# Kernel optimization log

Hardware: AMD Instinct MI355X
Metric: run time of the kernel (lower is better)

The kernel has to match this reference:

```python
import jax, jax.numpy as jnp
import numpy as np

B, C, T, F = 4, 96, 320, 256
BN_EPS = 1e-5


def _cbp(x, W, b, gamma, beta, mean, var, a):
    """1x1 Conv2d + BatchNorm2d (inference stats) + PReLU (single param)."""
    y = jnp.einsum('oc,bctf->botf', W, x) + b[None, :, None, None]
    scale = gamma * jax.lax.rsqrt(var + BN_EPS)
    y = (y - mean[None, :, None, None]) * scale[None, :, None, None] + beta[None, :, None, None]
    return jnp.where(y >= 0, y, a * y)


def setup_inputs() -> dict:
    key = jax.random.key(0)
    ks = jax.random.split(key, 24)
    d = {"inp": jax.random.normal(ks[0], (B, C, T, F), dtype=jnp.float32)}

    def mk_params(i, cout):
        kk = jax.random.split(ks[i], 7)
        return dict(
            W=jax.random.normal(kk[0], (cout, C), dtype=jnp.float32) / np.sqrt(C),
            b=jnp.zeros((cout,), dtype=jnp.float32),
            gamma=jnp.ones((cout,), dtype=jnp.float32) + 0.1 * jax.random.normal(kk[1], (cout,), dtype=jnp.float32),
            beta=0.1 * jax.random.normal(kk[2], (cout,), dtype=jnp.float32),
            mean=0.1 * jax.random.normal(kk[3], (cout,), dtype=jnp.float32),
            var=jax.random.uniform(kk[4], (cout,), dtype=jnp.float32) + 0.5,
            a=jnp.float32(0.25),
        )

    for tag, i, cout in (("f", 1, 3 * C), ("t", 2, 2 * C), ("p", 3, C)):
        p = mk_params(i, cout)
        for k, v in p.items():
            d[k + "_" + tag] = v
    return d


def reference(inp,
              W_f, b_f, gamma_f, beta_f, mean_f, var_f, a_f,
              W_t, b_t, gamma_t, beta_t, mean_t, var_t, a_t,
              W_p, b_p, gamma_p, beta_p, mean_p, var_p, a_p):
    c = inp.shape[1]
    scale = 1.0 / jnp.sqrt(jnp.float32(c))

    # frequency-axis attention
    f_qkv = _cbp(inp, W_f, b_f, gamma_f, beta_f, mean_f, var_f, a_f)  # [B,3C,T,F]
    qf, kf, v = f_qkv[:, :c], f_qkv[:, c:2 * c], f_qkv[:, 2 * c:]
    f_score = jnp.einsum('bctf,bcty->btfy', qf, kf) * scale
    f_score = jax.nn.softmax(f_score, axis=-1)
    f_out = jnp.einsum('btfy,bcty->bctf', f_score, v)

    # time-axis attention (NOTE: original's masked_fill is non-inplace and
    # its result is discarded, so the causal mask has NO effect; replicated.)
    t_qk = _cbp(inp, W_t, b_t, gamma_t, beta_t, mean_t, var_t, a_t)  # [B,2C,T,F]
    qt, kt = t_qk[:, :c], t_qk[:, c:]
    t_score = jnp.einsum('bctf,bcyf->bfty', qt, kt) * scale
    t_score = jax.nn.softmax(t_score, axis=-1)
    t_out = jnp.einsum('bfty,bcyf->bctf', t_score, f_out)

    out = _cbp(t_out, W_p, b_p, gamma_p, beta_p, mean_p, var_p, a_p)
    return out + inp
```

## Files before the change

### kernel.cpp

```cpp
#include <hip/hip_runtime.h>
#include <math.h>

typedef float f4 __attribute__((ext_vector_type(4)));
typedef float f2 __attribute__((ext_vector_type(2)));
typedef float f32x4 __attribute__((ext_vector_type(4)));
typedef _Float16 h8 __attribute__((ext_vector_type(8)));

constexpr int B_ = 4, C_ = 96, T_ = 320, F_ = 256;
constexpr int TF_ = T_ * F_;
constexpr float EPS_ = 1e-5f;
constexpr size_t QH_ = (size_t)C_ * TF_;

constexpr int WHF = 0, WLF = 27648, WHT = 55296, WLT = 73728,
              WHP = 92160, WLP = 101376, WTOT = 110592;

__global__ __launch_bounds__(256)
void prep_kernel(const float* __restrict__ Wf, const float* __restrict__ Wt,
                 const float* __restrict__ Wp,
                 const float* __restrict__ bf, const float* __restrict__ gf,
                 const float* __restrict__ bef, const float* __restrict__ mf,
                 const float* __restrict__ vf,
                 const float* __restrict__ bt, const float* __restrict__ gt,
                 const float* __restrict__ bet, const float* __restrict__ mt,
                 const float* __restrict__ vt,
                 const float* __restrict__ bp, const float* __restrict__ gp,
                 const float* __restrict__ bep, const float* __restrict__ mp,
                 const float* __restrict__ vp,
                 _Float16* __restrict__ wsp, float* __restrict__ scsh)
{
    const int gtid = blockIdx.x * 256 + threadIdx.x;
    const int gsz  = gridDim.x * 256;
    for (int i = gtid; i < 27648; i += gsz) {
        const float w = Wf[i]; const _Float16 h = (_Float16)w;
        wsp[WHF + i] = h; wsp[WLF + i] = (_Float16)(w - (float)h);
    }
    for (int i = gtid; i < 18432; i += gsz) {
        const float w = Wt[i]; const _Float16 h = (_Float16)w;
        wsp[WHT + i] = h; wsp[WLT + i] = (_Float16)(w - (float)h);
    }
    for (int i = gtid; i < 9216; i += gsz) {
        const float w = Wp[i]; const _Float16 h = (_Float16)w;
        wsp[WHP + i] = h; wsp[WLP + i] = (_Float16)(w - (float)h);
    }
    if (gtid < 288) {
        const float sc = gf[gtid] * rsqrtf(vf[gtid] + EPS_);
        scsh[2 * gtid] = sc;
        scsh[2 * gtid + 1] = fmaf(bf[gtid] - mf[gtid], sc, bef[gtid]);
    } else if (gtid < 480) {
        const int i = gtid - 288;
        const float sc = gt[i] * rsqrtf(vt[i] + EPS_);
        scsh[576 + 2 * i] = sc;
        scsh[576 + 2 * i + 1] = fmaf(bt[i] - mt[i], sc, bet[i]);
    } else if (gtid < 576) {
        const int i = gtid - 480;
        const float sc = gp[i] * rsqrtf(vp[i] + EPS_);
        scsh[960 + 2 * i] = sc;
        scsh[960 + 2 * i + 1] = fmaf(bp[i] - mp[i], sc, bep[i]);
    }
}

__global__ __launch_bounds__(256, 3)
void conv_ft(const float* __restrict__ x, const _Float16* __restrict__ wsp,
             const float* __restrict__ scsh,
             const float* __restrict__ aPf, const float* __restrict__ aPt,
             _Float16* __restrict__ yf, _Float16* __restrict__ yt,
             int bsx, int bsyf, int bsyt)
{
    constexpr int LS = 200;
    extern __shared__ _Float16 ldsh[];
    _Float16* Xs0 = ldsh;
    _Float16* Xs1 = ldsh + 64 * LS;

    x  += (size_t)blockIdx.y * bsx;
    yf += (size_t)blockIdx.y * bsyf;
    yt += (size_t)blockIdx.y * bsyt;

    const int tid = threadIdx.x;
    const int p0A = blockIdx.x * 128;
    const int p0B = p0A + 64;

    {
        const float* xg = x + p0A;
        for (int e = tid; e < 64 * 12; e += 256) {
            const int p = e & 63, k0 = (e >> 6) * 8;
            const float* xp = xg + (size_t)k0 * TF_ + p;
            h8 hv, lv;
#pragma unroll
            for (int j = 0; j < 8; ++j) {
                const float xv = xp[(size_t)j * TF_];
                const _Float16 xh = (_Float16)xv;
                hv[j] = xh;
                lv[j] = (_Float16)(xv - (float)xh);
            }
            *(h8*)&Xs0[p * LS + k0]      = hv;
            *(h8*)&Xs0[p * LS + 96 + k0] = lv;
        }
    }

    const int lane = tid & 63, wid = tid >> 6;
    const int l16 = lane & 15, lg = lane >> 4;
    const int wm = wid >> 1, wn = wid & 1;
    const float af_ = aPf[0], at_ = aPt[0];
    __syncthreads();

    float xpre[3][8];
#pragma unroll
    for (int it = 0; it < 3; ++it) {
        const int e = tid + it * 256;
        const int p = e & 63, k0 = (e >> 6) * 8;
        const float* xp = x + p0B + (size_t)k0 * TF_ + p;
#pragma unroll
        for (int j = 0; j < 8; ++j) xpre[it][j] = xp[(size_t)j * TF_];
    }

    auto compute5 = [&](const _Float16* Xs, int p0) {
#pragma unroll 1
        for (int cg = 0; cg < 5; ++cg) {
            const _Float16 *Wh, *Wl; const float* ss; float a; _Float16* yo;
            if (cg < 3) {
                Wh = wsp + WHF + cg * 9216;  Wl = wsp + WLF + cg * 9216;
                ss = scsh + cg * 192;        a = af_;
                yo = yf + (size_t)cg * QH_;
            } else {
                const int c2 = cg - 3;
                Wh = wsp + WHT + c2 * 9216;  Wl = wsp + WLT + c2 * 9216;
                ss = scsh + 576 + c2 * 192;  a = at_;
                yo = yt + (size_t)c2 * QH_;
            }

            f32x4 acc[3][2];
#pragma unroll
            for (int m = 0; m < 3; ++m)
#pragma unroll
                for (int n = 0; n < 2; ++n) acc[m][n] = (f32x4){0.f, 0.f, 0.f, 0.f};

#pragma unroll
            for (int kk = 0; kk < 3; ++kk) {
                h8 bfh[2], bfl[2];
#pragma unroll
                for (int n = 0; n < 2; ++n) {
                    const int prow = (wn * 2 + n) * 16 + l16;
                    bfh[n] = *(const h8*)&Xs[prow * LS + kk * 32 + lg * 8];
                    bfl[n] = *(const h8*)&Xs[prow * LS + 96 + kk * 32 + lg * 8];
                }
#pragma unroll
                for (int m = 0; m < 3; ++m) {
                    const int row = (wm * 3 + m) * 16 + l16;
                    const h8 wh = *(const h8*)&Wh[row * 96 + kk * 32 + lg * 8];
                    const h8 wl = *(const h8*)&Wl[row * 96 + kk * 32 + lg * 8];
#pragma unroll
                    for (int n = 0; n < 2; ++n) {
                        acc[m][n] = __builtin_amdgcn_mfma_f32_16x16x32_f16(wh, bfh[n], acc[m][n], 0, 0, 0);
                        acc[m][n] = __builtin_amdgcn_mfma_f32_16x16x32_f16(wl, bfh[n], acc[m][n], 0, 0, 0);
                        acc[m][n] = __builtin_amdgcn_mfma_f32_16x16x32_f16(wh, bfl[n], acc[m][n], 0, 0, 0);
                    }
                }
            }

#pragma unroll
            for (int m = 0; m < 3; ++m) {
#pragma unroll
                for (int r = 0; r < 4; ++r) {
                    const int col = (wm * 3 + m) * 16 + lg * 4 + r;
                    const f2 sp = *(const f2*)&ss[2 * col];
                    _Float16* yr = yo + (size_t)col * TF_ + p0 + wn * 32 + l16;
#pragma unroll
                    for (int n = 0; n < 2; ++n) {
                        const float v = fmaf(acc[m][n][r], sp[0], sp[1]);
                        yr[n * 16] = (_Float16)(v >= 0.f ? v : a * v);
                    }
                }
            }
        }
    };

    compute5(Xs0, p0A);

#pragma unroll
    for (int it = 0; it < 3; ++it) {
        const int e = tid + it * 256;
        const int p = e & 63, k0 = (e >> 6) * 8;
        h8 hv, lv;
#pragma unroll
        for (int j = 0; j < 8; ++j) {
            const _Float16 xh = (_Float16)xpre[it][j];
            hv[j] = xh;
            lv[j] = (_Float16)(xpre[it][j] - (float)xh);
        }
        *(h8*)&Xs1[p * LS + k0]      = hv;
        *(h8*)&Xs1[p * LS + 96 + k0] = lv;
    }
    __syncthreads();

    compute5(Xs1, p0B);
}

__global__ __launch_bounds__(256, 3)
void conv_p(const _Float16* __restrict__ x, const _Float16* __restrict__ wsp,
            const float* __restrict__ scsh, const float* __restrict__ aPp,
            _Float16* __restrict__ y, int bsx, int bsy)
{
    constexpr int LS = 104, PT = 160, NN = 5;
    extern __shared__ _Float16 ldsh[];
    _Float16* Xs = ldsh;

    x += (size_t)blockIdx.y * bsx;
    y += (size_t)blockIdx.y * bsy;

    const int tid = threadIdx.x;
    const int pt  = blockIdx.x & 1;
    const int g   = blockIdx.x >> 1;
    const int p0  = pt * PT;

    const _Float16* xg = x + (size_t)g * 96 * T_ + p0;
    for (int e = tid; e < PT * 12; e += 256) {
        const int p = e % PT, k0 = (e / PT) * 8;
        const _Float16* xp = xg + (size_t)k0 * T_ + p;
        h8 hv;
#pragma unroll
        for (int j = 0; j < 8; ++j) hv[j] = xp[(size_t)j * T_];
        *(h8*)&Xs[p * LS + k0] = hv;
    }

    const int lane = tid & 63, wid = tid >> 6;
    const int l16 = lane & 15, lg = lane >> 4;
    const int wm = wid >> 1, wn = wid & 1;
    const float a = aPp[0];
    const _Float16* Wh = wsp + WHP;
    const _Float16* Wl = wsp + WLP;
    const float* ss = scsh + 960;
    __syncthreads();

    f32x4 acc[3][NN];
#pragma unroll
    for (int m = 0; m < 3; ++m)
#pragma unroll
        for (int n = 0; n < NN; ++n) acc[m][n] = (f32x4){0.f, 0.f, 0.f, 0.f};

#pragma unroll
    for (int kk = 0; kk < 3; ++kk) {
        h8 bf[NN];
#pragma unroll
        for (int n = 0; n < NN; ++n)
            bf[n] = *(const h8*)&Xs[((wn * NN + n) * 16 + l16) * LS + kk * 32 + lg * 8];
#pragma unroll
        for (int m = 0; m < 3; ++m) {
            const int row = (wm * 3 + m) * 16 + l16;
            const h8 wh = *(const h8*)&Wh[row * 96 + kk * 32 + lg * 8];
            const h8 wl = *(const h8*)&Wl[row * 96 + kk * 32 + lg * 8];
#pragma unroll
            for (int n = 0; n < NN; ++n) {
                acc[m][n] = __builtin_amdgcn_mfma_f32_16x16x32_f16(wh, bf[n], acc[m][n], 0, 0, 0);
                acc[m][n] = __builtin_amdgcn_mfma_f32_16x16x32_f16(wl, bf[n], acc[m][n], 0, 0, 0);
            }
        }
    }

#pragma unroll
    for (int m = 0; m < 3; ++m) {
#pragma unroll
        for (int r = 0; r < 4; ++r) {
            const int col = (wm * 3 + m) * 16 + lg * 4 + r;
            const f2 sp = *(const f2*)&ss[2 * col];
            _Float16* yr = y + ((size_t)g * 96 + col) * T_ + p0 + wn * NN * 16 + l16;
#pragma unroll
            for (int n = 0; n < NN; ++n) {
                const float v = fmaf(acc[m][n][r], sp[0], sp[1]);
                yr[n * 16] = (_Float16)(v >= 0.f ? v : a * v);
            }
        }
    }
}

__device__ __forceinline__ void tr64_body(const _Float16* __restrict__ in,
                                          _Float16* __restrict__ out,
                                          int Mo, int No, int n0, int m0,
                                          _Float16* tile)
{
    const int t = threadIdx.x, ty = t >> 3, tx8 = t & 7;
#pragma unroll
    for (int r = 0; r < 2; ++r) {
        const int n = ty + r * 32;
        const h8 v = *(const h8*)&in[(size_t)(n0 + n) * Mo + m0 + tx8 * 8];
        const int c = tx8 ^ (n >> 3);
        *(h8*)&tile[n * 72 + c * 8] = v;
    }
    __syncthreads();
#pragma unroll
    for (int r = 0; r < 2; ++r) {
        const int mt = ty + r * 32;
        h8 v;
#pragma unroll
        for (int j = 0; j < 8; ++j) {
            const int n = tx8 * 8 + j;
            const int c = (mt >> 3) ^ tx8;
            v[j] = tile[n * 72 + c * 8 + (mt & 7)];
        }
        *(h8*)&out[(size_t)(m0 + mt) * No + n0 + tx8 * 8] = v;
    }
}

__global__ __launch_bounds__(256)
void transpose_trA(const _Float16* __restrict__ doh, _Float16* __restrict__ wsh)
{
    __shared__ _Float16 tile[64 * 72];
    const int b = blockIdx.z >> 1, t = blockIdx.z & 1;
    const _Float16* in  = t ? doh + (size_t)b * 2 * QH_
                            : wsh + (size_t)b * 3 * QH_;
    _Float16*       out = t ? wsh + (size_t)b * 3 * QH_ + 2 * QH_
                            : wsh + (size_t)b * 3 * QH_ + QH_;
    tr64_body(in, out, F_, C_ * T_, blockIdx.x * 64, blockIdx.y * 64, tile);
}

__global__ __launch_bounds__(256)
void transpose_trB(const _Float16* __restrict__ doh, _Float16* __restrict__ wsh)
{
    __shared__ _Float16 tile[64 * 72];
    const int b = blockIdx.z;
    tr64_body(doh + (size_t)b * 2 * QH_ + QH_, wsh + (size_t)b * 3 * QH_,
              F_, C_ * T_, blockIdx.x * 64, blockIdx.y * 64, tile);
}

__global__ __launch_bounds__(256)
void transpose_hf_res(const _Float16* __restrict__ in, const float* __restrict__ res,
                      float* __restrict__ out, int si, int sr, int so)
{
    __shared__ _Float16 tile[64 * 72];
    in  += (size_t)blockIdx.z * si;
    res += (size_t)blockIdx.z * sr;
    out += (size_t)blockIdx.z * so;
    const int n0 = blockIdx.x * 64, m0 = blockIdx.y * 64;
    const int t = threadIdx.x, ty = t >> 3, tx8 = t & 7;
#pragma unroll
    for (int r = 0; r < 2; ++r) {
        const int n = ty + r * 32;
        const h8 v = *(const h8*)&in[(size_t)(n0 + n) * (C_ * T_) + m0 + tx8 * 8];
        const int c = tx8 ^ (n >> 3);
        *(h8*)&tile[n * 72 + c * 8] = v;
    }
    __syncthreads();
#pragma unroll
    for (int r = 0; r < 2; ++r) {
        const int mt = ty + r * 32;
        const size_t obase = (size_t)(m0 + mt) * F_ + n0 + tx8 * 8;
        const f4 r0 = *(const f4*)&res[obase];
        const f4 r1 = *(const f4*)&res[obase + 4];
        f4 o0, o1;
#pragma unroll
        for (int j = 0; j < 8; ++j) {
            const int n = tx8 * 8 + j;
            const int c = (mt >> 3) ^ tx8;
            const float v = (float)tile[n * 72 + c * 8 + (mt & 7)];
            if (j < 4) o0[j] = v + r0[j]; else o1[j - 4] = v + r1[j - 4];
        }
        *(f4*)&out[obase]     = o0;
        *(f4*)&out[obase + 4] = o1;
    }
}

template<int MODE>
__global__ __launch_bounds__(256, 2)
void attn_mfma(const _Float16* __restrict__ Qb, const _Float16* __restrict__ Kb,
               const _Float16* __restrict__ Vb, _Float16* __restrict__ Ob,
               int qs, int ks, int vs, int os)
{
    constexpr int NY  = (MODE == 0) ? 256 : 320;
    constexpr int LD  = (MODE == 0) ? TF_ : T_;
    constexpr int NT  = NY / 16;
    constexpr int NYK = NY / 32;
    constexpr int KS  = 104;
    constexpr int VPS = NY + 24;
    constexpr int KVH = (NY * KS > 96 * VPS) ? NY * KS : 96 * VPS;
    constexpr int NG  = (MODE == 0) ? T_ : F_;
    constexpr int GOFF = (MODE == 0) ? F_ : C_ * T_;

    extern __shared__ _Float16 ldsh[];
    _Float16* KV = ldsh;
    _Float16* Pw = ldsh + KVH;

    const int lb    = blockIdx.y;
    const int strip = blockIdx.x / NG;
    const int grp   = blockIdx.x % NG;
    const int m0    = strip * 64;
    const size_t off = (size_t)grp * GOFF;
    const _Float16* Q = Qb + (size_t)lb * qs + off;
    const _Float16* K = Kb + (size_t)lb * ks + off;
    const _Float16* V = Vb + (size_t)lb * vs + off;
    _Float16*       O = Ob + (size_t)lb * os + off;

    const int tid  = threadIdx.x;
    const int lane = tid & 63, wid = tid >> 6;
    const int l16  = lane & 15, lg = lane >> 4;
    const int mw   = wid * 16;
    const float scale = 0.10206207261596575f;

    for (int e = tid; e < NY * 12; e += 256) {
        const int yy = e % NY, k0 = (e / NY) * 8;
        const _Float16* kp = K + (size_t)k0 * LD + yy;
        h8 hv;
#pragma unroll
        for (int j = 0; j < 8; ++j) hv[j] = kp[(size_t)j * LD];
        *(h8*)&KV[yy * KS + k0] = hv;
    }

    h8 aQ[3];
#pragma unroll
    for (int kk = 0; kk < 3; ++kk) {
        const _Float16* qp = Q + (size_t)(kk * 32 + lg * 8) * LD + m0 + mw + l16;
#pragma unroll
        for (int j = 0; j < 8; ++j) aQ[kk][j] = qp[(size_t)j * LD];
    }
    __syncthreads();

    f32x4 sacc[NT];
#pragma unroll
    for (int t = 0; t < NT; ++t) sacc[t] = (f32x4){0.f, 0.f, 0.f, 0.f};
#pragma unroll
    for (int kk = 0; kk < 3; ++kk) {
#pragma unroll
        for (int t = 0; t < NT; ++t) {
            const h8 bK = *(const h8*)&KV[(t * 16 + l16) * KS + kk * 32 + lg * 8];
            sacc[t] = __builtin_amdgcn_mfma_f32_16x16x32_f16(aQ[kk], bK, sacc[t], 0, 0, 0);
        }
    }

#pragma unroll
    for (int r = 0; r < 4; ++r) {
        float mx = sacc[0][r];
#pragma unroll
        for (int t = 1; t < NT; ++t) mx = fmaxf(mx, sacc[t][r]);
        for (int d = 1; d < 16; d <<= 1) mx = fmaxf(mx, __shfl_xor(mx, d));
        float pv[NT];
        float sum = 0.f;
#pragma unroll
        for (int t = 0; t < NT; ++t) {
            pv[t] = __expf((sacc[t][r] - mx) * scale); sum += pv[t];
        }
        for (int d = 1; d < 16; d <<= 1) sum += __shfl_xor(sum, d);
        const float inv = 1.f / sum;
#pragma unroll
        for (int t = 0; t < NT; ++t) sacc[t][r] = pv[t] * inv;
    }
    __syncthreads();

    constexpr int NY8 = NY / 8;
    for (int e = tid; e < 96 * NY8; e += 256) {
        const int c = e / NY8, y8 = e - c * NY8;
        *(h8*)&KV[c * VPS + y8 * 8] = *(const h8*)(V + (size_t)c * LD + y8 * 8);
    }
    __syncthreads();

    _Float16* Pme = Pw + wid * 640;
    f32x4 oacc[6];
#pragma unroll
    for (int ct = 0; ct < 6; ++ct) oacc[ct] = (f32x4){0.f, 0.f, 0.f, 0.f};

#pragma unroll
    for (int yk = 0; yk < NYK; ++yk) {
#pragma unroll
        for (int h = 0; h < 2; ++h)
#pragma unroll
            for (int r = 0; r < 4; ++r)
                Pme[(lg * 4 + r) * 40 + h * 16 + l16] = (_Float16)sacc[2 * yk + h][r];
        const h8 pf = *(const h8*)&Pme[l16 * 40 + lg * 8];
#pragma unroll
        for (int ct = 0; ct < 6; ++ct) {
            const h8 av = *(const h8*)&KV[(ct * 16 + l16) * VPS + yk * 32 + lg * 8];
            oacc[ct] = __builtin_amdgcn_mfma_f32_16x16x32_f16(av, pf, oacc[ct], 0, 0, 0);
        }
    }
#pragma unroll
    for (int ct = 0; ct < 6; ++ct)
#pragma unroll
        for (int r = 0; r < 4; ++r)
            O[(size_t)(ct * 16 + lg * 4 + r) * LD + m0 + mw + l16] = (_Float16)oacc[ct][r];
}

extern "C" void kernel_launch(void* const* d_in, const int* in_sizes, int n_in,
                              void* d_out, int out_size, void* d_ws, size_t ws_size,
                              hipStream_t stream)
{
    const float* inp = (const float*)d_in[0];
    const float* W_f = (const float*)d_in[1];  const float* b_f = (const float*)d_in[2];
    const float* g_f = (const float*)d_in[3];  const float* be_f = (const float*)d_in[4];
    const float* m_f = (const float*)d_in[5];  const float* v_f = (const float*)d_in[6];
    const float* a_f = (const float*)d_in[7];
    const float* W_t = (const float*)d_in[8];  const float* b_t = (const float*)d_in[9];
    const float* g_t = (const float*)d_in[10]; const float* be_t = (const float*)d_in[11];
    const float* m_t = (const float*)d_in[12]; const float* v_t = (const float*)d_in[13];
    const float* a_t = (const float*)d_in[14];
    const float* W_p = (const float*)d_in[15]; const float* b_p = (const float*)d_in[16];
    const float* g_p = (const float*)d_in[17]; const float* be_p = (const float*)d_in[18];
    const float* m_p = (const float*)d_in[19]; const float* v_p = (const float*)d_in[20];
    const float* a_p = (const float*)d_in[21];

    hipFuncSetAttribute((const void*)conv_ft,
                        hipFuncAttributeMaxDynamicSharedMemorySize, 51200);
    hipFuncSetAttribute((const void*)conv_p,
                        hipFuncAttributeMaxDynamicSharedMemorySize, 33280);
    hipFuncSetAttribute((const void*)attn_mfma<0>,
                        hipFuncAttributeMaxDynamicSharedMemorySize, 58880);
    hipFuncSetAttribute((const void*)attn_mfma<1>,
                        hipFuncAttributeMaxDynamicSharedMemorySize, 71680);

    constexpr int QH = (int)QH_;
    const size_t need4 = (size_t)12 * QH * 2 + (size_t)WTOT * 2 + 1152 * 4 + 4096;
    const int G = (ws_size >= need4) ? 4 : 2;

    _Float16* wsh  = (_Float16*)d_ws;
    _Float16* wsp  = wsh + (size_t)3 * G * QH;
    float*    scsh = (float*)(wsp + WTOT);

    prep_kernel<<<dim3(128), dim3(256), 0, stream>>>(
        W_f, W_t, W_p, b_f, g_f, be_f, m_f, v_f,
        b_t, g_t, be_t, m_t, v_t, b_p, g_p, be_p, m_p, v_p, wsp, scsh);

    for (int p = 0; p < B_ / G; ++p) {
        const float* xb  = inp + (size_t)p * G * QH;
        float*       dob = (float*)d_out + (size_t)p * G * QH;
        _Float16*    doh = (_Float16*)dob;

        conv_ft<<<dim3(640, G), dim3(256), 51200, stream>>>(
            xb, wsp, scsh, a_f, a_t, wsh, doh, QH, 3 * QH, 2 * QH);
        attn_mfma<0><<<dim3(T_ * (F_ / 64), G), dim3(256), 58880, stream>>>(
            wsh, wsh + QH_, wsh + 2 * QH_, wsh, 3 * QH, 3 * QH, 3 * QH, 3 * QH);
        transpose_trA<<<dim3(480, 4, 2 * G), dim3(256), 0, stream>>>(doh, wsh);
        transpose_trB<<<dim3(480, 4, G), dim3(256), 0, stream>>>(doh, wsh);
        attn_mfma<1><<<dim3(F_ * (T_ / 64), G), dim3(256), 71680, stream>>>(
            wsh + 2 * QH_, wsh, wsh + QH_, wsh + 2 * QH_,
            3 * QH, 3 * QH, 3 * QH, 3 * QH);
        conv_p<<<dim3(F_ * 2, G), dim3(256), 33280, stream>>>(
            wsh + 2 * QH_, wsp, scsh, a_p, wsh, 3 * QH, 3 * QH);
        transpose_hf_res<<<dim3(4, 480, G), dim3(256), 0, stream>>>(
            wsh, xb, dob, 3 * QH, QH, QH);
    }
}
```

Baseline: 713.7 us.

## Fuse time-axis attention with output 1x1 conv+BN+PReLU projection

Adds a fused kernel that runs the time-axis attention and then applies the projection conv (split-fp16 weights), BN scale/shift and PReLU straight from the attention output tile staged in shared memory. This removes the separate conv_p launch and the round trip of the attention output through global memory. It needs extra workspace (16 QH halves), and when that is not available it falls back to the old path. It also sets launch bounds of 2 blocks per CU with 70 KB of LDS, and adds register pressure from the epilogue.

```diff
diff --git a/kernel.cpp b/kernel.cpp
--- a/kernel.cpp
+++ b/kernel.cpp
@@ -476,6 +476,169 @@
             O[(size_t)(ct * 16 + lg * 4 + r) * LD + m0 + mw + l16] = (_Float16)oacc[ct][r];
 }
 
+__global__ __launch_bounds__(256, 2)
+void attn1_fused(const _Float16* __restrict__ Qb, const _Float16* __restrict__ Kb,
+                 const _Float16* __restrict__ Vb, _Float16* __restrict__ tmpb,
+                 const _Float16* __restrict__ wsp, const float* __restrict__ scsh,
+                 const float* __restrict__ aPp,
+                 int qs, int ks, int vs, int ts)
+{
+    constexpr int NY = 320, LD = T_, NT = 20, NYK = 10;
+    constexpr int KS = 104, VPS = 344;
+    constexpr int KVH = NY * KS;
+    constexpr int OS  = 104;
+
+    extern __shared__ _Float16 ldsh[];
+    _Float16* KV = ldsh;
+    _Float16* Pw = ldsh + KVH;
+    _Float16* Ot = ldsh;
+
+    const int lb    = blockIdx.y;
+    const int strip = blockIdx.x / F_;
+    const int grp   = blockIdx.x % F_;
+    const int m0    = strip * 64;
+    const size_t off = (size_t)grp * (C_ * T_);
+    const _Float16* Q = Qb + (size_t)lb * qs + off;
+    const _Float16* K = Kb + (size_t)lb * ks + off;
+    const _Float16* V = Vb + (size_t)lb * vs + off;
+    _Float16*     tmp = tmpb + (size_t)lb * ts + (size_t)grp * (96 * T_);
+
+    const int tid  = threadIdx.x;
+    const int lane = tid & 63, wid = tid >> 6;
+    const int l16  = lane & 15, lg = lane >> 4;
+    const int mw   = wid * 16;
+    const float scale = 0.10206207261596575f;
+
+    for (int e = tid; e < NY * 12; e += 256) {
+        const int yy = e % NY, k0 = (e / NY) * 8;
+        const _Float16* kp = K + (size_t)k0 * LD + yy;
+        h8 hv;
+#pragma unroll
+        for (int j = 0; j < 8; ++j) hv[j] = kp[(size_t)j * LD];
+        *(h8*)&KV[yy * KS + k0] = hv;
+    }
+
+    h8 aQ[3];
+#pragma unroll
+    for (int kk = 0; kk < 3; ++kk) {
+        const _Float16* qp = Q + (size_t)(kk * 32 + lg * 8) * LD + m0 + mw + l16;
+#pragma unroll
+        for (int j = 0; j < 8; ++j) aQ[kk][j] = qp[(size_t)j * LD];
+    }
+    __syncthreads();
+
+    f32x4 sacc[NT];
+#pragma unroll
+    for (int t = 0; t < NT; ++t) sacc[t] = (f32x4){0.f, 0.f, 0.f, 0.f};
+#pragma unroll
+    for (int kk = 0; kk < 3; ++kk) {
+#pragma unroll
+        for (int t = 0; t < NT; ++t) {
+            const h8 bK = *(const h8*)&KV[(t * 16 + l16) * KS + kk * 32 + lg * 8];
+            sacc[t] = __builtin_amdgcn_mfma_f32_16x16x32_f16(aQ[kk], bK, sacc[t], 0, 0, 0);
+        }
+    }
+
+#pragma unroll
+    for (int r = 0; r < 4; ++r) {
+        float mx = sacc[0][r];
+#pragma unroll
+        for (int t = 1; t < NT; ++t) mx = fmaxf(mx, sacc[t][r]);
+        for (int d = 1; d < 16; d <<= 1) mx = fmaxf(mx, __shfl_xor(mx, d));
+        float pv[NT];
+        float sum = 0.f;
+#pragma unroll
+        for (int t = 0; t < NT; ++t) {
+            pv[t] = __expf((sacc[t][r] - mx) * scale); sum += pv[t];
+        }
+        for (int d = 1; d < 16; d <<= 1) sum += __shfl_xor(sum, d);
+        const float inv = 1.f / sum;
+#pragma unroll
+        for (int t = 0; t < NT; ++t) sacc[t][r] = pv[t] * inv;
+    }
+    __syncthreads();
+
+    for (int e = tid; e < 96 * 40; e += 256) {
+        const int c = e / 40, y8 = e - c * 40;
+        *(h8*)&KV[c * VPS + y8 * 8] = *(const h8*)(V + (size_t)c * LD + y8 * 8);
+    }
+    __syncthreads();
+
+    _Float16* Pme = Pw + wid * 640;
+    f32x4 oacc[6];
+#pragma unroll
+    for (int ct = 0; ct < 6; ++ct) oacc[ct] = (f32x4){0.f, 0.f, 0.f, 0.f};
+
+#pragma unroll
+    for (int yk = 0; yk < NYK; ++yk) {
+#pragma unroll
+        for (int h = 0; h < 2; ++h)
+#pragma unroll
+            for (int r = 0; r < 4; ++r)
+                Pme[(lg * 4 + r) * 40 + h * 16 + l16] = (_Float16)sacc[2 * yk + h][r];
+        const h8 pf = *(const h8*)&Pme[l16 * 40 + lg * 8];
+#pragma unroll
+        for (int ct = 0; ct < 6; ++ct) {
+            const h8 av = *(const h8*)&KV[(ct * 16 + l16) * VPS + yk * 32 + lg * 8];
+            oacc[ct] = __builtin_amdgcn_mfma_f32_16x16x32_f16(av, pf, oacc[ct], 0, 0, 0);
+        }
+    }
+
+    __syncthreads();
+#pragma unroll
+    for (int ct = 0; ct < 6; ++ct)
+#pragma unroll
+        for (int r = 0; r < 4; ++r)
+            Ot[(mw + l16) * OS + ct * 16 + lg * 4 + r] = (_Float16)oacc[ct][r];
+    __syncthreads();
+
+    const int wm = wid >> 1, wn = wid & 1;
+    const float a = aPp[0];
+    const _Float16* Wh = wsp + WHP;
+    const _Float16* Wl = wsp + WLP;
+    const float* ss = scsh + 960;
+
+    f32x4 acc2[3][2];
+#pragma unroll
+    for (int m = 0; m < 3; ++m)
+#pragma unroll
+        for (int n = 0; n < 2; ++n) acc2[m][n] = (f32x4){0.f, 0.f, 0.f, 0.f};
+
+#pragma unroll
+    for (int kk = 0; kk < 3; ++kk) {
+        h8 bf[2];
+#pragma unroll
+        for (int n = 0; n < 2; ++n)
+            bf[n] = *(const h8*)&Ot[((wn * 2 + n) * 16 + l16) * OS + kk * 32 + lg * 8];
+#pragma unroll
+        for (int m = 0; m < 3; ++m) {
+            const int row = (wm * 3 + m) * 16 + l16;
+            const h8 wh = *(const h8*)&Wh[row * 96 + kk * 32 + lg * 8];
+            const h8 wl = *(const h8*)&Wl[row * 96 + kk * 32 + lg * 8];
+#pragma unroll
+            for (int n = 0; n < 2; ++n) {
+                acc2[m][n] = __builtin_amdgcn_mfma_f32_16x16x32_f16(wh, bf[n], acc2[m][n], 0, 0, 0);
+                acc2[m][n] = __builtin_amdgcn_mfma_f32_16x16x32_f16(wl, bf[n], acc2[m][n], 0, 0, 0);
+            }
+        }
+    }
+
+#pragma unroll
+    for (int m = 0; m < 3; ++m) {
+#pragma unroll
+        for (int r = 0; r < 4; ++r) {
+            const int co = (wm * 3 + m) * 16 + lg * 4 + r;
+            const f2 sp = *(const f2*)&ss[2 * co];
+            _Float16* yr = tmp + (size_t)co * T_ + m0 + wn * 32 + l16;
+#pragma unroll
+            for (int n = 0; n < 2; ++n) {
+                const float v = fmaf(acc2[m][n][r], sp[0], sp[1]);
+                yr[n * 16] = (_Float16)(v >= 0.f ? v : a * v);
+            }
+        }
+    }
+}
+
 extern "C" void kernel_launch(void* const* d_in, const int* in_sizes, int n_in,
                               void* d_out, int out_size, void* d_ws, size_t ws_size,
                               hipStream_t stream)
@@ -502,14 +665,20 @@
                         hipFuncAttributeMaxDynamicSharedMemorySize, 58880);
     hipFuncSetAttribute((const void*)attn_mfma<1>,
                         hipFuncAttributeMaxDynamicSharedMemorySize, 71680);
+    hipFuncSetAttribute((const void*)attn1_fused,
+                        hipFuncAttributeMaxDynamicSharedMemorySize, 71680);
 
     constexpr int QH = (int)QH_;
-    const size_t need4 = (size_t)12 * QH * 2 + (size_t)WTOT * 2 + 1152 * 4 + 4096;
+    const size_t tail  = (size_t)WTOT * 2 + 1152 * 4 + 4096;
+    const size_t need4 = (size_t)12 * QH * 2 + tail;
+    const size_t need16 = (size_t)16 * QH * 2 + tail;
     const int G = (ws_size >= need4) ? 4 : 2;
+    const bool FUSED = (G == 4) && (ws_size >= need16);
 
     _Float16* wsh  = (_Float16*)d_ws;
-    _Float16* wsp  = wsh + (size_t)3 * G * QH;
+    _Float16* wsp  = wsh + (size_t)(3 * G + (FUSED ? 4 : 0)) * QH;
     float*    scsh = (float*)(wsp + WTOT);
+    _Float16* tmpf = wsh + (size_t)3 * G * QH;
 
     prep_kernel<<<dim3(128), dim3(256), 0, stream>>>(
         W_f, W_t, W_p, b_f, g_f, be_f, m_f, v_f,
@@ -526,12 +695,21 @@
             wsh, wsh + QH_, wsh + 2 * QH_, wsh, 3 * QH, 3 * QH, 3 * QH, 3 * QH);
         transpose_trA<<<dim3(480, 4, 2 * G), dim3(256), 0, stream>>>(doh, wsh);
         transpose_trB<<<dim3(480, 4, G), dim3(256), 0, stream>>>(doh, wsh);
-        attn_mfma<1><<<dim3(F_ * (T_ / 64), G), dim3(256), 71680, stream>>>(
-            wsh + 2 * QH_, wsh, wsh + QH_, wsh + 2 * QH_,
-            3 * QH, 3 * QH, 3 * QH, 3 * QH);
-        conv_p<<<dim3(F_ * 2, G), dim3(256), 33280, stream>>>(
-            wsh + 2 * QH_, wsp, scsh, a_p, wsh, 3 * QH, 3 * QH);
-        transpose_hf_res<<<dim3(4, 480, G), dim3(256), 0, stream>>>(
-            wsh, xb, dob, 3 * QH, QH, QH);
-    }
-}
+
+        if (FUSED) {
+            attn1_fused<<<dim3(F_ * (T_ / 64), G), dim3(256), 71680, stream>>>(
+                wsh + 2 * QH_, wsh, wsh + QH_, tmpf, wsp, scsh, a_p,
+                3 * QH, 3 * QH, 3 * QH, QH);
+            transpose_hf_res<<<dim3(4, 480, G), dim3(256), 0, stream>>>(
+                tmpf, xb, dob, QH, QH, QH);
+        } else {
+            attn_mfma<1><<<dim3(F_ * (T_ / 64), G), dim3(256), 71680, stream>>>(
+                wsh + 2 * QH_, wsh, wsh + QH_, wsh + 2 * QH_,
+                3 * QH, 3 * QH, 3 * QH, 3 * QH);
+            conv_p<<<dim3(F_ * 2, G), dim3(256), 33280, stream>>>(
+                wsh + 2 * QH_, wsp, scsh, a_p, wsh, 3 * QH, 3 * QH);
+            transpose_hf_res<<<dim3(4, 480, G), dim3(256), 0, stream>>>(
+                wsh, xb, dob, 3 * QH, QH, QH);
+        }
+    }
+}
```

New measurement: 712.8 us. Within noise of the previous version (-0.1%).
